# Kernel tuning notes

Hardware: AMD Instinct MI355X
Metric: run time of the kernel (lower is better)

## Reference

```python
import jax, jax.numpy as jnp
import numpy as np
import math

B, H, W, CIN = 4, 64, 64, 256
G, C, K = 8, 32, 9
MAX_SCALE = 6.0


def setup_inputs() -> dict:
    key = jax.random.key(0)
    ks = jax.random.split(key, 10)
    s = 0.02
    x = jax.random.normal(ks[0], (B, H, W, CIN), dtype=jnp.float32)
    # linear params stored as [in, out]
    v_w = jax.random.normal(ks[1], (CIN, G * C), dtype=jnp.float32) * s
    v_b = jax.random.normal(ks[2], (G * C,), dtype=jnp.float32) * s
    qd_w = jax.random.normal(ks[3], (CIN, G * K * 2), dtype=jnp.float32) * s
    qd_b = jax.random.normal(ks[4], (G * K * 2,), dtype=jnp.float32) * s
    qs_w = jax.random.normal(ks[5], (CIN, G * K), dtype=jnp.float32) * s  # no bias
    qw_w = jax.random.normal(ks[6], (CIN, G * K), dtype=jnp.float32) * s
    qw_b = jax.random.normal(ks[7], (G * K,), dtype=jnp.float32) * s
    out_w = jax.random.normal(ks[8], (G * C, CIN), dtype=jnp.float32) * s
    out_b = jax.random.normal(ks[9], (CIN,), dtype=jnp.float32) * s
    # deformables_prior: 3x3 grid in [-1,1], meshgrid indexing='xy', stacked (x,y)
    n = int(math.isqrt(K))
    d = np.linspace(-1.0, 1.0, n, dtype=np.float32)
    gx, gy = np.meshgrid(d, d, indexing='xy')
    prior = jnp.asarray(np.stack([gx, gy], axis=-1).reshape(1, 1, 1, 1, K, 2))
    # deformables_scale: per-group inverse-sigmoid of (i+1)/G - 1e-4
    sc = np.array([(i + 1) / G - 1e-4 for i in range(G)], dtype=np.float32)
    dscale = jnp.asarray(np.log(sc / (1.0 - sc)).reshape(1, 1, 1, G, 1, 1))
    return dict(x=x, v_w=v_w, v_b=v_b, qd_w=qd_w, qd_b=qd_b, qs_w=qs_w,
                qw_w=qw_w, qw_b=qw_b, out_w=out_w, out_b=out_b,
                prior=prior, dscale=dscale)


def _dcn_sample(v, deform, weights):
    # v: [B,H,W,G,C]; deform: [B,H,W,G,K,2] pixel offsets (x,y); weights: [B,H,W,G,K]
    b_, h_, w_, g_, c_ = v.shape
    ww = jnp.arange(w_, dtype=v.dtype)[None, None, :, None, None]
    hh = jnp.arange(h_, dtype=v.dtype)[None, :, None, None, None]
    px = ww + deform[..., 0]  # [B,H,W,G,K]
    py = hh + deform[..., 1]
    x0 = jnp.floor(px); y0 = jnp.floor(py)
    wx1 = px - x0; wx0 = 1.0 - wx1
    wy1 = py - y0; wy0 = 1.0 - wy1
    bidx = jnp.arange(b_)[:, None, None, None, None]
    gidx = jnp.arange(g_)[None, None, None, :, None]

    def gather(yi, xi):
        valid = ((yi >= 0) & (yi < h_) & (xi >= 0) & (xi < w_)).astype(v.dtype)
        yc = jnp.clip(yi, 0, h_ - 1).astype(jnp.int32)
        xc = jnp.clip(xi, 0, w_ - 1).astype(jnp.int32)
        return v[bidx, yc, xc, gidx] * valid[..., None]  # [B,H,W,G,K,C]

    samp = (gather(y0, x0) * (wy0 * wx0)[..., None]
            + gather(y0, x0 + 1) * (wy0 * wx1)[..., None]
            + gather(y0 + 1, x0) * (wy1 * wx0)[..., None]
            + gather(y0 + 1, x0 + 1) * (wy1 * wx1)[..., None])
    # weighted sum over kernels -> [B,H,W,G,C]
    return jnp.einsum('bhwgkc,bhwgk->bhwgc', samp, weights)


def reference(x, v_w, v_b, qd_w, qd_b, qs_w, qw_w, qw_b, out_w, out_b, prior, dscale):
    b_, h_, w_, _ = x.shape
    v = (x @ v_w + v_b).reshape(b_, h_, w_, G, C)
    deform = (x @ qd_w + qd_b).reshape(b_, h_, w_, G, K, 2)
    scale = (x @ qs_w).reshape(b_, h_, w_, G, K, 1) + dscale
    deform = (deform + prior) * jax.nn.sigmoid(scale) * MAX_SCALE
    weights = (x @ qw_w + qw_b).reshape(b_, h_, w_, G, K)
    out = _dcn_sample(v, deform, weights)  # [B,H,W,G,C]
    out = out.reshape(b_, h_, w_, G * C)
    return out @ out_w + out_b
```

## Files before the change

### kernel.cpp

```cpp
#include <hip/hip_runtime.h>
#include <hip/hip_fp16.h>

#define NPIX 16384

typedef __attribute__((ext_vector_type(8))) short short8;
typedef __attribute__((ext_vector_type(8))) _Float16 half8;
typedef __attribute__((ext_vector_type(4))) float f32x4;

__device__ __forceinline__ unsigned short f2bf(float f) {
    unsigned u = __float_as_uint(f);
    unsigned r = (u + 0x7fffu + ((u >> 16) & 1u)) >> 16;
    return (unsigned short)r;
}
__device__ __forceinline__ unsigned short f2h_us(float f) {
    union { _Float16 h; unsigned short u; } cv;
    cv.h = (_Float16)f;
    return cv.u;
}
__device__ __forceinline__ unsigned hdup(float f) {
    unsigned short u = f2h_us(f);
    return (unsigned)u | ((unsigned)u << 16);
}
__device__ __forceinline__ unsigned hfma2u(unsigned w, unsigned v, unsigned a) {
    union { unsigned u; __half2 h; } W, V, A, R;
    W.u = w; V.u = v; A.u = a;
    R.h = __hfma2(W.h, V.h, A.h);
    return R.u;
}
__device__ __forceinline__ unsigned hadd2u(unsigned a, unsigned b) {
    union { unsigned u; __half2 h; } A, B, R;
    A.u = a; B.u = b;
    R.h = __hadd2(A.h, B.h);
    return R.u;
}

#define GLOAD16(SRC, DST) \
    __builtin_amdgcn_global_load_lds( \
        (const __attribute__((address_space(1))) unsigned*)(SRC), \
        (__attribute__((address_space(3))) unsigned*)(DST), 16, 0, 0)

__device__ __forceinline__ float wsrc(int k, int n,
    const float* v_w, const float* qd_w, const float* qs_w,
    const float* qw_w, const float* out_w)
{
    if (n < 256) return v_w[k * 256 + n];
    n -= 256;
    if (n < 144) return qd_w[k * 144 + n];
    n -= 144;
    if (n < 72)  return qs_w[k * 72 + n];
    n -= 72;
    if (n < 72)  return qw_w[k * 72 + n];
    n -= 72;
    if (n < 32)  return 0.f;
    return out_w[k * 256 + (n - 32)];
}

__global__ __launch_bounds__(256) void prep_all(
    const float* __restrict__ x, unsigned short* __restrict__ xb,
    const float* __restrict__ v_w, const float* __restrict__ qd_w,
    const float* __restrict__ qs_w, const float* __restrict__ qw_w,
    const float* __restrict__ out_w, const float* __restrict__ qd_b,
    const float* __restrict__ qw_b,
    unsigned short* __restrict__ Wt, float* __restrict__ biasD,
    unsigned short* __restrict__ vpad)
{
    __shared__ float t[64][65];
    const int bid = blockIdx.x;
    const int tid = threadIdx.x;

    if (bid < 2048) {
        const int bb = (bid >> 3) + (bid & 7) * 256;
        const size_t i = (size_t)bb * 256 + tid;
        const float4 v0 = *(const float4*)(x + i * 8);
        const float4 v1 = *(const float4*)(x + i * 8 + 4);
        uint4 pk;
        pk.x = f2bf(v0.x) | ((unsigned)f2bf(v0.y) << 16);
        pk.y = f2bf(v0.z) | ((unsigned)f2bf(v0.w) << 16);
        pk.z = f2bf(v1.x) | ((unsigned)f2bf(v1.y) << 16);
        pk.w = f2bf(v1.z) | ((unsigned)f2bf(v1.w) << 16);
        *(uint4*)(xb + i * 8) = pk;
        return;
    }
    if (bid == 2100) {
        for (int i = tid; i < 320; i += 256) {
            float bv = 0.f;
            if (i < 144)                  bv = qd_b[i];
            else if (i >= 216 && i < 288) bv = qw_b[i - 216];
            biasD[i] = bv;
        }
        for (int i = tid; i < 512; i += 256) vpad[i] = 0;
        return;
    }
    const int tile = bid - 2048;
    const int tn = tile % 13;
    const int tk = tile / 13;
    #pragma unroll
    for (int i = 0; i < 16; ++i) {
        const int idx = tid + i * 256;
        const int r = idx >> 6;
        const int c = idx & 63;
        t[r][c] = wsrc(tk * 64 + r, tn * 64 + c, v_w, qd_w, qs_w, qw_w, out_w);
    }
    __syncthreads();
    const bool asF16 = (tn >= 9);
    #pragma unroll
    for (int i = 0; i < 8; ++i) {
        const int idx = tid + i * 256;
        const int rn = idx >> 5;
        const int cc = idx & 31;
        unsigned pk;
        if (asF16)
            pk = (unsigned)f2h_us(t[cc * 2][rn]) | ((unsigned)f2h_us(t[cc * 2 + 1][rn]) << 16);
        else
            pk = (unsigned)f2bf(t[cc * 2][rn]) | ((unsigned)f2bf(t[cc * 2 + 1][rn]) << 16);
        ((unsigned*)(Wt + (size_t)(tn * 64 + rn) * 256 + tk * 64))[cc] = pk;
    }
}

__global__ __launch_bounds__(256) void gemm_proj(
    const unsigned short* __restrict__ A, const unsigned short* __restrict__ Wt,
    const float* __restrict__ v_b, const float* __restrict__ biasD,
    unsigned short* __restrict__ v_bf, float* __restrict__ proj)
{
    __shared__ unsigned short As[64 * 256];
    __shared__ unsigned short Bs[64 * 256];

    const int tid  = threadIdx.x;
    const int wid  = tid >> 6;
    const int lane = tid & 63;
    const int bx   = blockIdx.x;
    const int tile = (bx >> 3) + (bx & 7) * 32;
    const int row0 = tile * 64;
    const int j    = blockIdx.y;

    const unsigned short* Ab = A  + (size_t)row0 * 256;
    const unsigned short* Bb = Wt + (size_t)(j * 64) * 256;
    const int rl = lane >> 5;
    const int gl = lane & 31;

    #pragma unroll
    for (int it = 0; it < 8; ++it) {
        const int r   = wid * 16 + it * 2 + rl;
        const int gsw = gl ^ (r & 7);
        GLOAD16(Ab + r * 256 + gsw * 8, &As[(wid * 16 + it * 2) * 256]);
        GLOAD16(Bb + r * 256 + gsw * 8, &Bs[(wid * 16 + it * 2) * 256]);
    }
    asm volatile("s_waitcnt vmcnt(0)" ::: "memory");
    __syncthreads();

    f32x4 acc00 = {0,0,0,0}, acc01 = {0,0,0,0};
    f32x4 acc10 = {0,0,0,0}, acc11 = {0,0,0,0};

    const int wr = (wid >> 1) * 32;
    const int wc = (wid & 1) * 32;
    const int fr = lane & 15;
    const int fg = lane >> 4;

    const int ra0 = wr + fr, ra1 = ra0 + 16;
    const int rb0 = wc + fr, rb1 = rb0 + 16;
    const int sa  = ra0 & 7;
    const int sb  = rb0 & 7;

    #pragma unroll
    for (int t = 0; t < 8; ++t) {
        const int gran = t * 4 + fg;
        short8 a0 = *(const short8*)&As[ra0 * 256 + (gran ^ sa) * 8];
        short8 a1 = *(const short8*)&As[ra1 * 256 + (gran ^ sa) * 8];
        short8 b0 = *(const short8*)&Bs[rb0 * 256 + (gran ^ sb) * 8];
        short8 b1 = *(const short8*)&Bs[rb1 * 256 + (gran ^ sb) * 8];
        acc00 = __builtin_amdgcn_mfma_f32_16x16x32_bf16(a0, b0, acc00, 0, 0, 0);
        acc01 = __builtin_amdgcn_mfma_f32_16x16x32_bf16(a0, b1, acc01, 0, 0, 0);
        acc10 = __builtin_amdgcn_mfma_f32_16x16x32_bf16(a1, b0, acc10, 0, 0, 0);
        acc11 = __builtin_amdgcn_mfma_f32_16x16x32_bf16(a1, b1, acc11, 0, 0, 0);
    }

    if (j < 4) {
        const int colA = j * 64 + wc + fr;
        const int colB = colA + 16;
        const int gA = colA >> 5, cA = colA & 31;
        const int gB = colB >> 5, cB = colB & 31;
        const float biasA = v_b[colA];
        const float biasB = v_b[colB];
        #pragma unroll
        for (int jj = 0; jj < 4; ++jj) {
            const int r0a = row0 + wr + fg * 4 + jj;
            const int r1a = r0a + 16;
            const int b0i = r0a >> 12;
            const int hw0 = r0a & 4095, hw1 = r1a & 4095;
            v_bf[((size_t)(b0i * 8 + gA) * 4096 + hw0) * 32 + cA] = f2h_us(acc00[jj] + biasA);
            v_bf[((size_t)(b0i * 8 + gB) * 4096 + hw0) * 32 + cB] = f2h_us(acc01[jj] + biasB);
            v_bf[((size_t)(b0i * 8 + gA) * 4096 + hw1) * 32 + cA] = f2h_us(acc10[jj] + biasA);
            v_bf[((size_t)(b0i * 8 + gB) * 4096 + hw1) * 32 + cB] = f2h_us(acc11[jj] + biasB);
        }
    } else {
        const int colA = (j - 4) * 64 + wc + fr;
        const int colB = colA + 16;
        const float biasA = biasD[colA];
        const float biasB = biasD[colB];
        #pragma unroll
        for (int jj = 0; jj < 4; ++jj) {
            const int r0a = row0 + wr + fg * 4 + jj;
            const int r1a = r0a + 16;
            proj[(size_t)r0a * 320 + colA] = acc00[jj] + biasA;
            proj[(size_t)r0a * 320 + colB] = acc01[jj] + biasB;
            proj[(size_t)r1a * 320 + colA] = acc10[jj] + biasA;
            proj[(size_t)r1a * 320 + colB] = acc11[jj] + biasB;
        }
    }
}

__global__ __launch_bounds__(256) void gemm_out(
    const unsigned short* __restrict__ A, const unsigned short* __restrict__ WtO,
    const float* __restrict__ bias, float* __restrict__ Y)
{
    __shared__ unsigned short As[64 * 256];
    __shared__ unsigned short Bs[64 * 256];

    const int tid  = threadIdx.x;
    const int wid  = tid >> 6;
    const int lane = tid & 63;
    const int bx   = blockIdx.x;
    const int tile = (bx >> 3) + (bx & 7) * 32;
    const int row0 = tile * 64;
    const int col0 = blockIdx.y * 64;

    const unsigned short* Ab = A   + (size_t)row0 * 256;
    const unsigned short* Bb = WtO + (size_t)col0 * 256;
    const int rl = lane >> 5;
    const int gl = lane & 31;

    #pragma unroll
    for (int it = 0; it < 8; ++it) {
        const int r   = wid * 16 + it * 2 + rl;
        const int gsw = gl ^ (r & 7);
        GLOAD16(Ab + r * 256 + gsw * 8, &As[(wid * 16 + it * 2) * 256]);
        GLOAD16(Bb + r * 256 + gsw * 8, &Bs[(wid * 16 + it * 2) * 256]);
    }
    asm volatile("s_waitcnt vmcnt(0)" ::: "memory");
    __syncthreads();

    f32x4 acc00 = {0,0,0,0}, acc01 = {0,0,0,0};
    f32x4 acc10 = {0,0,0,0}, acc11 = {0,0,0,0};

    const int wr = (wid >> 1) * 32;
    const int wc = (wid & 1) * 32;
    const int fr = lane & 15;
    const int fg = lane >> 4;

    const int ra0 = wr + fr, ra1 = ra0 + 16;
    const int rb0 = wc + fr, rb1 = rb0 + 16;
    const int sa  = ra0 & 7;
    const int sb  = rb0 & 7;

    #pragma unroll
    for (int t = 0; t < 8; ++t) {
        const int gran = t * 4 + fg;
        half8 a0 = *(const half8*)&As[ra0 * 256 + (gran ^ sa) * 8];
        half8 a1 = *(const half8*)&As[ra1 * 256 + (gran ^ sa) * 8];
        half8 b0 = *(const half8*)&Bs[rb0 * 256 + (gran ^ sb) * 8];
        half8 b1 = *(const half8*)&Bs[rb1 * 256 + (gran ^ sb) * 8];
        acc00 = __builtin_amdgcn_mfma_f32_16x16x32_f16(a0, b0, acc00, 0, 0, 0);
        acc01 = __builtin_amdgcn_mfma_f32_16x16x32_f16(a0, b1, acc01, 0, 0, 0);
        acc10 = __builtin_amdgcn_mfma_f32_16x16x32_f16(a1, b0, acc10, 0, 0, 0);
        acc11 = __builtin_amdgcn_mfma_f32_16x16x32_f16(a1, b1, acc11, 0, 0, 0);
    }

    const int colA = col0 + wc + fr;
    const int colB = colA + 16;
    const float biasA = bias[colA];
    const float biasB = bias[colB];
    #pragma unroll
    for (int jj = 0; jj < 4; ++jj) {
        const int r0a = row0 + wr + fg * 4 + jj;
        const int r1a = r0a + 16;
        Y[(size_t)r0a * 256 + colA] = acc00[jj] + biasA;
        Y[(size_t)r0a * 256 + colB] = acc01[jj] + biasB;
        Y[(size_t)r1a * 256 + colA] = acc10[jj] + biasA;
        Y[(size_t)r1a * 256 + colB] = acc11[jj] + biasB;
    }
}

__global__ __launch_bounds__(256) void dcn_sample7(
    const unsigned short* __restrict__ vbuf,
    const float* __restrict__ proj,
    const float* __restrict__ prior,
    const float* __restrict__ dscale,
    unsigned short* __restrict__ mid)
{
    __shared__ int      offs[576 * 2];
    __shared__ unsigned wpk [576 * 4];

    const int tid = threadIdx.x;
    const int bid  = blockIdx.x;
    const int wg   = (bid & 7) * 256 + (bid >> 3);
    const int pix0 = wg * 8;

    for (int it = tid; it < 576; it += 256) {
        const int p   = it / 72;
        const int rem = it - p * 72;
        const int g   = rem / 9;
        const int k   = rem - g * 9;
        const int pix = pix0 + p;
        const int b   = pix >> 12;
        const int hw  = pix & 4095;
        const int h   = hw >> 6, w = hw & 63;

        const float* row = proj + (size_t)pix * 320;
        const float qdx = row[g * 18 + k * 2 + 0];
        const float qdy = row[g * 18 + k * 2 + 1];
        const float s   = row[144 + g * 9 + k] + dscale[g];
        const float wt  = row[216 + g * 9 + k];
        const float sig6 = 6.0f / (1.0f + __expf(-s));
        const float px = (float)w + (qdx + prior[k * 2 + 0]) * sig6;
        const float py = (float)h + (qdy + prior[k * 2 + 1]) * sig6;

        const float x0f = floorf(px), y0f = floorf(py);
        const int ix = (int)x0f, iy = (int)y0f;
        const float wx1 = px - x0f, wx0 = 1.f - wx1;
        const float wy1 = py - y0f, wy0 = 1.f - wy1;
        const int plane = (b * 8 + g) << 12;

        const bool vy0 = (iy >= 0) & (iy < 64);
        const bool vy1 = (iy >= -1) & (iy < 63);
        const bool vx0 = (ix >= 0) & (ix < 64);
        const bool vx1 = (ix >= -1) & (ix < 63);
        const float w00 = (vy0 & vx0) ? wt * wy0 * wx0 : 0.f;
        const float w10 = (vy1 & vx0) ? wt * wy1 * wx0 : 0.f;
        const float w01 = (vy0 & vx1) ? wt * wy0 * wx1 : 0.f;
        const float w11 = (vy1 & vx1) ? wt * wy1 * wx1 : 0.f;
        wpk[it * 4 + 0] = hdup(w00);
        wpk[it * 4 + 1] = hdup(w10);
        wpk[it * 4 + 2] = hdup(w01);
        wpk[it * 4 + 3] = hdup(w11);

        const int xs  = min(max(ix,     -1), 63);
        const int y0c = min(max(iy,      0), 63);
        const int y1c = min(max(iy + 1,  0), 63);
        offs[it * 2 + 0] = (plane + y0c * 64 + xs) * 64;
        offs[it * 2 + 1] = (plane + y1c * 64 + xs) * 64;
    }
    __syncthreads();

    const int p4 = tid >> 6;
    const int g  = (tid >> 3) & 7;
    const int q  = tid & 7;
    const int xh = q >> 2;
    const int qb = q * 16;
    const char* vbb = (const char*)vbuf;

    unsigned aA0=0,aA1=0,aA2=0,aA3=0, aB0=0,aB1=0,aB2=0,aB3=0;
    unsigned bA0=0,bA1=0,bA2=0,bA3=0, bB0=0,bB1=0,bB2=0,bB3=0;
    const int item0a = p4 * 72 + g * 9;
    const int item0b = (p4 + 4) * 72 + g * 9;

    #pragma unroll
    for (int k = 0; k < 9; ++k) {
        {
            const int it = item0a + k;
            const int2  o2 = *(const int2*)&offs[it * 2];
            const uint2 wp = *(const uint2*)&wpk[it * 4 + xh * 2];
            const uint4 r0 = *(const uint4*)(vbb + o2.x + qb);
            const uint4 r1 = *(const uint4*)(vbb + o2.y + qb);
            aA0 = hfma2u(wp.x, r0.x, aA0);
            aA1 = hfma2u(wp.x, r0.y, aA1);
            aA2 = hfma2u(wp.x, r0.z, aA2);
            aA3 = hfma2u(wp.x, r0.w, aA3);
            aB0 = hfma2u(wp.y, r1.x, aB0);
            aB1 = hfma2u(wp.y, r1.y, aB1);
            aB2 = hfma2u(wp.y, r1.z, aB2);
            aB3 = hfma2u(wp.y, r1.w, aB3);
        }
        {
            const int it = item0b + k;
            const int2  o2 = *(const int2*)&offs[it * 2];
            const uint2 wp = *(const uint2*)&wpk[it * 4 + xh * 2];
            const uint4 r0 = *(const uint4*)(vbb + o2.x + qb);
            const uint4 r1 = *(const uint4*)(vbb + o2.y + qb);
            bA0 = hfma2u(wp.x, r0.x, bA0);
            bA1 = hfma2u(wp.x, r0.y, bA1);
            bA2 = hfma2u(wp.x, r0.z, bA2);
            bA3 = hfma2u(wp.x, r0.w, bA3);
            bB0 = hfma2u(wp.y, r1.x, bB0);
            bB1 = hfma2u(wp.y, r1.y, bB1);
            bB2 = hfma2u(wp.y, r1.z, bB2);
            bB3 = hfma2u(wp.y, r1.w, bB3);
        }
    }

    uint4 oA, oB;
    {
        unsigned c;
        c = hadd2u(aA0, aB0); c = hadd2u(c, (unsigned)__shfl_xor((int)c, 4)); oA.x = c;
        c = hadd2u(aA1, aB1); c = hadd2u(c, (unsigned)__shfl_xor((int)c, 4)); oA.y = c;
        c = hadd2u(aA2, aB2); c = hadd2u(c, (unsigned)__shfl_xor((int)c, 4)); oA.z = c;
        c = hadd2u(aA3, aB3); c = hadd2u(c, (unsigned)__shfl_xor((int)c, 4)); oA.w = c;
        c = hadd2u(bA0, bB0); c = hadd2u(c, (unsigned)__shfl_xor((int)c, 4)); oB.x = c;
        c = hadd2u(bA1, bB1); c = hadd2u(c, (unsigned)__shfl_xor((int)c, 4)); oB.y = c;
        c = hadd2u(bA2, bB2); c = hadd2u(c, (unsigned)__shfl_xor((int)c, 4)); oB.z = c;
        c = hadd2u(bA3, bB3); c = hadd2u(c, (unsigned)__shfl_xor((int)c, 4)); oB.w = c;
    }
    if (xh == 0) {
        const int cq8 = (q & 3) * 8;
        *(uint4*)(mid + (size_t)(pix0 + p4) * 256 + g * 32 + cq8) = oA;
        *(uint4*)(mid + (size_t)(pix0 + p4 + 4) * 256 + g * 32 + cq8) = oB;
    }
}

extern "C" void kernel_launch(void* const* d_in, const int* in_sizes, int n_in,
                              void* d_out, int out_size, void* d_ws, size_t ws_size,
                              hipStream_t stream)
{
    (void)in_sizes; (void)n_in; (void)out_size; (void)ws_size;

    const float* x      = (const float*)d_in[0];
    const float* v_w    = (const float*)d_in[1];
    const float* v_b    = (const float*)d_in[2];
    const float* qd_w   = (const float*)d_in[3];
    const float* qd_b   = (const float*)d_in[4];
    const float* qs_w   = (const float*)d_in[5];
    const float* qw_w   = (const float*)d_in[6];
    const float* qw_b   = (const float*)d_in[7];
    const float* out_w  = (const float*)d_in[8];
    const float* out_b  = (const float*)d_in[9];
    const float* prior  = (const float*)d_in[10];
    const float* dscale = (const float*)d_in[11];
    float* out = (float*)d_out;

    char* ws = (char*)d_ws;
    unsigned short* xb    = (unsigned short*)(ws);
    unsigned short* v_bf  = (unsigned short*)(ws + 8388608);
    unsigned short* vpad  = (unsigned short*)(ws + 16777216);
    float*          proj  = (float*)(ws + 16778240);
    unsigned short* mid   = (unsigned short*)(ws + 37749760);
    unsigned short* Wt    = (unsigned short*)(ws + 46138368);
    float*          biasD = (float*)(ws + 46564352);

    prep_all<<<dim3(2101), dim3(256), 0, stream>>>(x, xb, v_w, qd_w, qs_w, qw_w,
                                                   out_w, qd_b, qw_b, Wt, biasD, vpad);

    gemm_proj<<<dim3(256, 9), dim3(256), 0, stream>>>(xb, Wt, v_b, biasD, v_bf, proj);

    dcn_sample7<<<dim3(NPIX / 8), dim3(256), 0, stream>>>(v_bf, proj, prior, dscale, mid);

    gemm_out<<<dim3(256, 4), dim3(256), 0, stream>>>(mid, Wt + 576 * 256, out_b, out);
}
```

Measured before the change: 56.33 us.

## Fuse deformable sampling with output projection GEMM via shared-memory tile

Merges the sampling kernel and the output GEMM into one kernel. Each 8-pixel block writes its sampled features into a zero-padded 16-row shared tile, and four waves each compute 64 output columns with MFMA, reading weights straight from global memory. This removes the mid buffer round trip through global memory and one kernel launch. In exchange, half of each MFMA's rows are padding, and every block re-reads the full 128KB output weight matrix from L2 without LDS staging.

```diff
diff --git a/kernel.cpp b/kernel.cpp
--- a/kernel.cpp
+++ b/kernel.cpp
@@ -209,91 +209,25 @@
     }
 }
 
-__global__ __launch_bounds__(256) void gemm_out(
-    const unsigned short* __restrict__ A, const unsigned short* __restrict__ WtO,
-    const float* __restrict__ bias, float* __restrict__ Y)
-{
-    __shared__ unsigned short As[64 * 256];
-    __shared__ unsigned short Bs[64 * 256];
-
-    const int tid  = threadIdx.x;
-    const int wid  = tid >> 6;
-    const int lane = tid & 63;
-    const int bx   = blockIdx.x;
-    const int tile = (bx >> 3) + (bx & 7) * 32;
-    const int row0 = tile * 64;
-    const int col0 = blockIdx.y * 64;
-
-    const unsigned short* Ab = A   + (size_t)row0 * 256;
-    const unsigned short* Bb = WtO + (size_t)col0 * 256;
-    const int rl = lane >> 5;
-    const int gl = lane & 31;
-
-    #pragma unroll
-    for (int it = 0; it < 8; ++it) {
-        const int r   = wid * 16 + it * 2 + rl;
-        const int gsw = gl ^ (r & 7);
-        GLOAD16(Ab + r * 256 + gsw * 8, &As[(wid * 16 + it * 2) * 256]);
-        GLOAD16(Bb + r * 256 + gsw * 8, &Bs[(wid * 16 + it * 2) * 256]);
-    }
-    asm volatile("s_waitcnt vmcnt(0)" ::: "memory");
-    __syncthreads();
-
-    f32x4 acc00 = {0,0,0,0}, acc01 = {0,0,0,0};
-    f32x4 acc10 = {0,0,0,0}, acc11 = {0,0,0,0};
-
-    const int wr = (wid >> 1) * 32;
-    const int wc = (wid & 1) * 32;
-    const int fr = lane & 15;
-    const int fg = lane >> 4;
-
-    const int ra0 = wr + fr, ra1 = ra0 + 16;
-    const int rb0 = wc + fr, rb1 = rb0 + 16;
-    const int sa  = ra0 & 7;
-    const int sb  = rb0 & 7;
-
-    #pragma unroll
-    for (int t = 0; t < 8; ++t) {
-        const int gran = t * 4 + fg;
-        half8 a0 = *(const half8*)&As[ra0 * 256 + (gran ^ sa) * 8];
-        half8 a1 = *(const half8*)&As[ra1 * 256 + (gran ^ sa) * 8];
-        half8 b0 = *(const half8*)&Bs[rb0 * 256 + (gran ^ sb) * 8];
-        half8 b1 = *(const half8*)&Bs[rb1 * 256 + (gran ^ sb) * 8];
-        acc00 = __builtin_amdgcn_mfma_f32_16x16x32_f16(a0, b0, acc00, 0, 0, 0);
-        acc01 = __builtin_amdgcn_mfma_f32_16x16x32_f16(a0, b1, acc01, 0, 0, 0);
-        acc10 = __builtin_amdgcn_mfma_f32_16x16x32_f16(a1, b0, acc10, 0, 0, 0);
-        acc11 = __builtin_amdgcn_mfma_f32_16x16x32_f16(a1, b1, acc11, 0, 0, 0);
-    }
-
-    const int colA = col0 + wc + fr;
-    const int colB = colA + 16;
-    const float biasA = bias[colA];
-    const float biasB = bias[colB];
-    #pragma unroll
-    for (int jj = 0; jj < 4; ++jj) {
-        const int r0a = row0 + wr + fg * 4 + jj;
-        const int r1a = r0a + 16;
-        Y[(size_t)r0a * 256 + colA] = acc00[jj] + biasA;
-        Y[(size_t)r0a * 256 + colB] = acc01[jj] + biasB;
-        Y[(size_t)r1a * 256 + colA] = acc10[jj] + biasA;
-        Y[(size_t)r1a * 256 + colB] = acc11[jj] + biasB;
-    }
-}
-
-__global__ __launch_bounds__(256) void dcn_sample7(
+__global__ __launch_bounds__(256) void dcn_fused(
     const unsigned short* __restrict__ vbuf,
     const float* __restrict__ proj,
     const float* __restrict__ prior,
     const float* __restrict__ dscale,
-    unsigned short* __restrict__ mid)
+    const unsigned short* __restrict__ WtO,
+    const float* __restrict__ out_b,
+    float* __restrict__ out)
 {
     __shared__ int      offs[576 * 2];
     __shared__ unsigned wpk [576 * 4];
+    __shared__ unsigned short mid_s[16 * 264];
 
     const int tid = threadIdx.x;
     const int bid  = blockIdx.x;
     const int wg   = (bid & 7) * 256 + (bid >> 3);
     const int pix0 = wg * 8;
+
+    for (int i = tid; i < 528; i += 256) ((uint4*)mid_s)[i] = make_uint4(0,0,0,0);
 
     for (int it = tid; it < 576; it += 256) {
         const int p   = it / 72;
@@ -341,68 +275,110 @@
     }
     __syncthreads();
 
-    const int p4 = tid >> 6;
-    const int g  = (tid >> 3) & 7;
-    const int q  = tid & 7;
-    const int xh = q >> 2;
-    const int qb = q * 16;
-    const char* vbb = (const char*)vbuf;
-
-    unsigned aA0=0,aA1=0,aA2=0,aA3=0, aB0=0,aB1=0,aB2=0,aB3=0;
-    unsigned bA0=0,bA1=0,bA2=0,bA3=0, bB0=0,bB1=0,bB2=0,bB3=0;
-    const int item0a = p4 * 72 + g * 9;
-    const int item0b = (p4 + 4) * 72 + g * 9;
-
-    #pragma unroll
-    for (int k = 0; k < 9; ++k) {
+    {
+        const int p4 = tid >> 6;
+        const int g  = (tid >> 3) & 7;
+        const int q  = tid & 7;
+        const int xh = q >> 2;
+        const int qb = q * 16;
+        const char* vbb = (const char*)vbuf;
+
+        unsigned aA0=0,aA1=0,aA2=0,aA3=0, aB0=0,aB1=0,aB2=0,aB3=0;
+        unsigned bA0=0,bA1=0,bA2=0,bA3=0, bB0=0,bB1=0,bB2=0,bB3=0;
+        const int item0a = p4 * 72 + g * 9;
+        const int item0b = (p4 + 4) * 72 + g * 9;
+
+        #pragma unroll
+        for (int k = 0; k < 9; ++k) {
+            {
+                const int it = item0a + k;
+                const int2  o2 = *(const int2*)&offs[it * 2];
+                const uint2 wp = *(const uint2*)&wpk[it * 4 + xh * 2];
+                const uint4 r0 = *(const uint4*)(vbb + o2.x + qb);
+                const uint4 r1 = *(const uint4*)(vbb + o2.y + qb);
+                aA0 = hfma2u(wp.x, r0.x, aA0);
+                aA1 = hfma2u(wp.x, r0.y, aA1);
+                aA2 = hfma2u(wp.x, r0.z, aA2);
+                aA3 = hfma2u(wp.x, r0.w, aA3);
+                aB0 = hfma2u(wp.y, r1.x, aB0);
+                aB1 = hfma2u(wp.y, r1.y, aB1);
+                aB2 = hfma2u(wp.y, r1.z, aB2);
+                aB3 = hfma2u(wp.y, r1.w, aB3);
+            }
+            {
+                const int it = item0b + k;
+                const int2  o2 = *(const int2*)&offs[it * 2];
+                const uint2 wp = *(const uint2*)&wpk[it * 4 + xh * 2];
+                const uint4 r0 = *(const uint4*)(vbb + o2.x + qb);
+                const uint4 r1 = *(const uint4*)(vbb + o2.y + qb);
+                bA0 = hfma2u(wp.x, r0.x, bA0);
+                bA1 = hfma2u(wp.x, r0.y, bA1);
+                bA2 = hfma2u(wp.x, r0.z, bA2);
+                bA3 = hfma2u(wp.x, r0.w, bA3);
+                bB0 = hfma2u(wp.y, r1.x, bB0);
+                bB1 = hfma2u(wp.y, r1.y, bB1);
+                bB2 = hfma2u(wp.y, r1.z, bB2);
+                bB3 = hfma2u(wp.y, r1.w, bB3);
+            }
+        }
+
+        uint4 oA, oB;
         {
-            const int it = item0a + k;
-            const int2  o2 = *(const int2*)&offs[it * 2];
-            const uint2 wp = *(const uint2*)&wpk[it * 4 + xh * 2];
-            const uint4 r0 = *(const uint4*)(vbb + o2.x + qb);
-            const uint4 r1 = *(const uint4*)(vbb + o2.y + qb);
-            aA0 = hfma2u(wp.x, r0.x, aA0);
-            aA1 = hfma2u(wp.x, r0.y, aA1);
-            aA2 = hfma2u(wp.x, r0.z, aA2);
-            aA3 = hfma2u(wp.x, r0.w, aA3);
-            aB0 = hfma2u(wp.y, r1.x, aB0);
-            aB1 = hfma2u(wp.y, r1.y, aB1);
-            aB2 = hfma2u(wp.y, r1.z, aB2);
-            aB3 = hfma2u(wp.y, r1.w, aB3);
-        }
-        {
-            const int it = item0b + k;
-            const int2  o2 = *(const int2*)&offs[it * 2];
-            const uint2 wp = *(const uint2*)&wpk[it * 4 + xh * 2];
-            const uint4 r0 = *(const uint4*)(vbb + o2.x + qb);
-            const uint4 r1 = *(const uint4*)(vbb + o2.y + qb);
-            bA0 = hfma2u(wp.x, r0.x, bA0);
-            bA1 = hfma2u(wp.x, r0.y, bA1);
-            bA2 = hfma2u(wp.x, r0.z, bA2);
-            bA3 = hfma2u(wp.x, r0.w, bA3);
-            bB0 = hfma2u(wp.y, r1.x, bB0);
-            bB1 = hfma2u(wp.y, r1.y, bB1);
-            bB2 = hfma2u(wp.y, r1.z, bB2);
-            bB3 = hfma2u(wp.y, r1.w, bB3);
-        }
-    }
-
-    uint4 oA, oB;
+            unsigned c;
+            c = hadd2u(aA0, aB0); c = hadd2u(c, (unsigned)__shfl_xor((int)c, 4)); oA.x = c;
+            c = hadd2u(aA1, aB1); c = hadd2u(c, (unsigned)__shfl_xor((int)c, 4)); oA.y = c;
+            c = hadd2u(aA2, aB2); c = hadd2u(c, (unsigned)__shfl_xor((int)c, 4)); oA.z = c;
+            c = hadd2u(aA3, aB3); c = hadd2u(c, (unsigned)__shfl_xor((int)c, 4)); oA.w = c;
+            c = hadd2u(bA0, bB0); c = hadd2u(c, (unsigned)__shfl_xor((int)c, 4)); oB.x = c;
+            c = hadd2u(bA1, bB1); c = hadd2u(c, (unsigned)__shfl_xor((int)c, 4)); oB.y = c;
+            c = hadd2u(bA2, bB2); c = hadd2u(c, (unsigned)__shfl_xor((int)c, 4)); oB.z = c;
+            c = hadd2u(bA3, bB3); c = hadd2u(c, (unsigned)__shfl_xor((int)c, 4)); oB.w = c;
+        }
+        if (xh == 0) {
+            const int cq8 = (q & 3) * 8;
+            *(uint4*)&mid_s[(p4    ) * 264 + g * 32 + cq8] = oA;
+            *(uint4*)&mid_s[(p4 + 4) * 264 + g * 32 + cq8] = oB;
+        }
+    }
+    __syncthreads();
+
     {
-        unsigned c;
-        c = hadd2u(aA0, aB0); c = hadd2u(c, (unsigned)__shfl_xor((int)c, 4)); oA.x = c;
-        c = hadd2u(aA1, aB1); c = hadd2u(c, (unsigned)__shfl_xor((int)c, 4)); oA.y = c;
-        c = hadd2u(aA2, aB2); c = hadd2u(c, (unsigned)__shfl_xor((int)c, 4)); oA.z = c;
-        c = hadd2u(aA3, aB3); c = hadd2u(c, (unsigned)__shfl_xor((int)c, 4)); oA.w = c;
-        c = hadd2u(bA0, bB0); c = hadd2u(c, (unsigned)__shfl_xor((int)c, 4)); oB.x = c;
-        c = hadd2u(bA1, bB1); c = hadd2u(c, (unsigned)__shfl_xor((int)c, 4)); oB.y = c;
-        c = hadd2u(bA2, bB2); c = hadd2u(c, (unsigned)__shfl_xor((int)c, 4)); oB.z = c;
-        c = hadd2u(bA3, bB3); c = hadd2u(c, (unsigned)__shfl_xor((int)c, 4)); oB.w = c;
-    }
-    if (xh == 0) {
-        const int cq8 = (q & 3) * 8;
-        *(uint4*)(mid + (size_t)(pix0 + p4) * 256 + g * 32 + cq8) = oA;
-        *(uint4*)(mid + (size_t)(pix0 + p4 + 4) * 256 + g * 32 + cq8) = oB;
+        const int wv = tid >> 6;
+        const int ln = tid & 63;
+        const int fr = ln & 15;
+        const int fg = ln >> 4;
+        const int col0 = wv * 64;
+
+        f32x4 acc0 = {0,0,0,0}, acc1 = {0,0,0,0}, acc2 = {0,0,0,0}, acc3 = {0,0,0,0};
+
+        #pragma unroll
+        for (int t = 0; t < 8; ++t) {
+            const half8 a = *(const half8*)&mid_s[fr * 264 + t * 32 + fg * 8];
+            const half8 b0 = *(const half8*)(WtO + (size_t)(col0 + 0  + fr) * 256 + t * 32 + fg * 8);
+            const half8 b1 = *(const half8*)(WtO + (size_t)(col0 + 16 + fr) * 256 + t * 32 + fg * 8);
+            const half8 b2 = *(const half8*)(WtO + (size_t)(col0 + 32 + fr) * 256 + t * 32 + fg * 8);
+            const half8 b3 = *(const half8*)(WtO + (size_t)(col0 + 48 + fr) * 256 + t * 32 + fg * 8);
+            acc0 = __builtin_amdgcn_mfma_f32_16x16x32_f16(a, b0, acc0, 0, 0, 0);
+            acc1 = __builtin_amdgcn_mfma_f32_16x16x32_f16(a, b1, acc1, 0, 0, 0);
+            acc2 = __builtin_amdgcn_mfma_f32_16x16x32_f16(a, b2, acc2, 0, 0, 0);
+            acc3 = __builtin_amdgcn_mfma_f32_16x16x32_f16(a, b3, acc3, 0, 0, 0);
+        }
+
+        if (fg < 2) {
+            const float bias0 = out_b[col0 + 0  + fr];
+            const float bias1 = out_b[col0 + 16 + fr];
+            const float bias2 = out_b[col0 + 32 + fr];
+            const float bias3 = out_b[col0 + 48 + fr];
+            #pragma unroll
+            for (int jj = 0; jj < 4; ++jj) {
+                const int row = fg * 4 + jj;
+                float* orow = out + (size_t)(pix0 + row) * 256 + col0;
+                orow[0  + fr] = acc0[jj] + bias0;
+                orow[16 + fr] = acc1[jj] + bias1;
+                orow[32 + fr] = acc2[jj] + bias2;
+                orow[48 + fr] = acc3[jj] + bias3;
+            }
+        }
     }
 }
 
@@ -431,7 +407,6 @@
     unsigned short* v_bf  = (unsigned short*)(ws + 8388608);
     unsigned short* vpad  = (unsigned short*)(ws + 16777216);
     float*          proj  = (float*)(ws + 16778240);
-    unsigned short* mid   = (unsigned short*)(ws + 37749760);
     unsigned short* Wt    = (unsigned short*)(ws + 46138368);
     float*          biasD = (float*)(ws + 46564352);
 
@@ -440,7 +415,6 @@
 
     gemm_proj<<<dim3(256, 9), dim3(256), 0, stream>>>(xb, Wt, v_b, biasD, v_bf, proj);
 
-    dcn_sample7<<<dim3(NPIX / 8), dim3(256), 0, stream>>>(v_bf, proj, prior, dscale, mid);
-
-    gemm_out<<<dim3(256, 4), dim3(256), 0, stream>>>(mid, Wt + 576 * 256, out_b, out);
-}
+    dcn_fused<<<dim3(NPIX / 8), dim3(256), 0, stream>>>(v_bf, proj, prior, dscale,
+                                                        Wt + 576 * 256, out_b, out);
+}
```

After: 74.78 us. +32.8%, slower.
